# Optimization experiments

Measured on AMD Instinct MI355X. Metric: run time of the kernel, lower is better.

Reference implementation:

```python
import jax, jax.numpy as jnp
import numpy as np

B, S, D_MODEL = 4, 2048, 1024
H, DK, DV = 16, 64, 64
MASKED = False


def setup_inputs() -> dict:
    key = jax.random.key(0)
    ks = jax.random.split(key, 7)
    return {
        "q": jax.random.normal(ks[0], (B, S, D_MODEL), dtype=jnp.float32),
        "k": jax.random.normal(ks[1], (B, S, D_MODEL), dtype=jnp.float32),
        "v": jax.random.normal(ks[2], (B, S, D_MODEL), dtype=jnp.float32),
        "Wq": jax.random.normal(ks[3], (H, D_MODEL, DK), dtype=jnp.float32) * 0.05,
        "Wk": jax.random.normal(ks[4], (H, D_MODEL, DK), dtype=jnp.float32) * 0.05,
        "Wv": jax.random.normal(ks[5], (H, D_MODEL, DV), dtype=jnp.float32) * 0.05,
        "Wo": jax.random.normal(ks[6], (H * DV, D_MODEL), dtype=jnp.float32) * 0.05,
    }


def reference(q, k, v, Wq, Wk, Wv, Wo):
    # Per-head projections, batched over heads instead of a Python loop.
    Q = jnp.einsum("bsd,hdk->bhsk", q, Wq)  # [B,H,S,Dk]
    K = jnp.einsum("btd,hdk->bhtk", k, Wk)  # [B,H,S,Dk]
    V = jnp.einsum("btd,hdv->bhtv", v, Wv)  # [B,H,S,Dv]

    scale = 1.0 / jnp.sqrt(jnp.asarray(DK, dtype=Q.dtype))
    scores = jnp.einsum("bhsk,bhtk->bhst", Q, K) * scale  # [B,H,S,S]
    if MASKED:
        causal = jnp.tril(jnp.ones((S, S), dtype=bool))
        scores = jnp.where(causal, scores, jnp.finfo(scores.dtype).min)
    attn = jax.nn.softmax(scores, axis=-1)
    heads = jnp.einsum("bhst,bhtv->bhsv", attn, V)  # [B,H,S,Dv]

    # concat heads along feature dim (tf.concat(heads, axis=-1)) then Wo projection
    multi = heads.transpose(0, 2, 1, 3).reshape(q.shape[0], q.shape[1], H * DV)
    return multi @ Wo  # [B,S,D_MODEL]
```

## Files before the change

### kernel.cpp

```cpp
#include <hip/hip_runtime.h>
#include <hip/hip_bf16.h>

typedef __attribute__((ext_vector_type(8))) short short8;
typedef __attribute__((ext_vector_type(4))) short short4v;
typedef __attribute__((ext_vector_type(4))) float f32x4;
typedef __attribute__((ext_vector_type(2))) float f32x2;
typedef __attribute__((ext_vector_type(4))) unsigned short us4;
typedef __attribute__((ext_vector_type(2))) unsigned int u32x2;

#define NB 4
#define SEQ 2048
#define DMODEL 1024
#define NH 16
#define DHEAD 64
#define QSCALE 0.18033688011112042f
#define FM 34.0f

static __device__ __forceinline__ unsigned short f2bf(float f) {
    __hip_bfloat16 h = __float2bfloat16(f);
    return *reinterpret_cast<unsigned short*>(&h);
}
static __device__ __forceinline__ unsigned int cvt_pk(float lo, float hi) {
    float2 t; t.x = lo; t.y = hi;
    __hip_bfloat162 h = __float22bfloat162_rn(t);
    return *reinterpret_cast<unsigned int*>(&h);
}

typedef __attribute__((address_space(3))) unsigned int lds_u32_t;
typedef __attribute__((address_space(1))) const unsigned int glob_u32_t;
static __device__ __forceinline__ void gl_lds16(const unsigned short* g, unsigned short* l) {
    __builtin_amdgcn_global_load_lds((glob_u32_t*)g, (lds_u32_t*)l, 16, 0, 0);
}

__global__ __launch_bounds__(256) void prep_all(const float* __restrict__ q,
                                                const float* __restrict__ k,
                                                const float* __restrict__ v,
                                                const float* __restrict__ wq,
                                                const float* __restrict__ wk,
                                                const float* __restrict__ wv,
                                                const float* __restrict__ wo,
                                                unsigned short* __restrict__ xq,
                                                unsigned short* __restrict__ xk,
                                                unsigned short* __restrict__ xv,
                                                unsigned short* __restrict__ oq,
                                                unsigned short* __restrict__ ok,
                                                unsigned short* __restrict__ ov,
                                                unsigned short* __restrict__ oo) {
    const int z = blockIdx.y;
    int i = blockIdx.x * 256 + threadIdx.x;
    if (z < 3) {
        const float* in = z == 0 ? q : (z == 1 ? k : v);
        unsigned short* out = z == 0 ? xq : (z == 1 ? xk : xv);
        f32x4 val = ((const f32x4*)in)[i];
        u32x2 o;
        o.x = cvt_pk(val.x, val.y);
        o.y = cvt_pk(val.z, val.w);
        ((u32x2*)out)[i] = o;
    } else {
        if (i >= NH * DMODEL * DHEAD) return;
        if (z < 6) {
            const float* w = z == 3 ? wq : (z == 4 ? wk : wv);
            unsigned short* out = z == 3 ? oq : (z == 4 ? ok : ov);
            float scale = z == 3 ? QSCALE : 1.0f;
            int kk = i & 63;
            int d  = (i >> 6) & 1023;
            int h  = i >> 16;
            out[(size_t)(h * 64 + kk) * DMODEL + d] = f2bf(w[i] * scale);
        } else {
            int c = i & 1023;
            int r = i >> 10;
            oo[(size_t)c * 1024 + r] = f2bf(wo[i]);
        }
    }
}

struct GemmAcc { f32x4 a[4][4]; };

static __device__ __forceinline__ void gemm_core(const unsigned short* __restrict__ A,
                                                 const unsigned short* __restrict__ Bt,
                                                 unsigned short (*As)[4096],
                                                 unsigned short (*Bs)[4096],
                                                 int m0, int n0, int K, GemmAcc& acc) {
    const int tid = threadIdx.x;
    const int w = tid >> 6, l = tid & 63;
    const int lane16 = l & 15, quad = l >> 4;
    const int wr = w >> 1, wc = w & 1;

#pragma unroll
    for (int a = 0; a < 4; a++)
#pragma unroll
        for (int b = 0; b < 4; b++) acc.a[a][b] = (f32x4){0.f, 0.f, 0.f, 0.f};

    const int i0 = 2 * w, i1 = 2 * w + 1;
    const int rs = l >> 2;
    const int cc = ((l & 3) ^ ((l >> 3) & 3)) * 8;
    const unsigned short* a0 = A + (size_t)(m0 + i0 * 16 + rs) * K + cc;
    const unsigned short* a1 = A + (size_t)(m0 + i1 * 16 + rs) * K + cc;
    const unsigned short* b0 = Bt + (size_t)(n0 + i0 * 16 + rs) * K + cc;
    const unsigned short* b1 = Bt + (size_t)(n0 + i1 * 16 + rs) * K + cc;

    const int cl = (quad ^ ((lane16 >> 1) & 3)) * 8;
    const int ra = (wr * 64 + lane16) * 32 + cl;
    const int rb = (wc * 64 + lane16) * 32 + cl;

    for (int k0 = 0; k0 < K; k0 += 64) {
        __syncthreads();
#pragma unroll
        for (int h = 0; h < 2; h++) {
            gl_lds16(a0 + k0 + h * 32, &As[h][i0 * 512]);
            gl_lds16(a1 + k0 + h * 32, &As[h][i1 * 512]);
            gl_lds16(b0 + k0 + h * 32, &Bs[h][i0 * 512]);
            gl_lds16(b1 + k0 + h * 32, &Bs[h][i1 * 512]);
        }
        __syncthreads();
#pragma unroll
        for (int h = 0; h < 2; h++) {
            short8 af[4], bf[4];
#pragma unroll
            for (int mt = 0; mt < 4; mt++) af[mt] = *(const short8*)&As[h][ra + mt * 512];
#pragma unroll
            for (int nt = 0; nt < 4; nt++) bf[nt] = *(const short8*)&Bs[h][rb + nt * 512];
#pragma unroll
            for (int mt = 0; mt < 4; mt++)
#pragma unroll
                for (int nt = 0; nt < 4; nt++)
                    acc.a[mt][nt] = __builtin_amdgcn_mfma_f32_16x16x32_bf16(
                        af[mt], bf[nt], acc.a[mt][nt], 0, 0, 0);
        }
    }
}

__global__ __launch_bounds__(256) void gemm_qkv(const unsigned short* __restrict__ xq,
                                                const unsigned short* __restrict__ xk,
                                                const unsigned short* __restrict__ xv,
                                                const unsigned short* __restrict__ wq,
                                                const unsigned short* __restrict__ wk,
                                                const unsigned short* __restrict__ wv,
                                                unsigned short* __restrict__ Qb,
                                                unsigned short* __restrict__ Kb,
                                                unsigned short* __restrict__ Vtb) {
    __shared__ unsigned short As[2][4096];
    __shared__ unsigned short Bs[2][4096];
    const int z = blockIdx.z;
    const unsigned short* A = z == 0 ? xq : (z == 1 ? xk : xv);
    const unsigned short* Bt = z == 0 ? wq : (z == 1 ? wk : wv);
    unsigned short* out = z == 0 ? Qb : (z == 1 ? Kb : Vtb);

    const int m0 = blockIdx.x * 128, n0 = blockIdx.y * 128;
    GemmAcc acc;
    gemm_core(A, Bt, As, Bs, m0, n0, DMODEL, acc);

    const int l = threadIdx.x & 63, w = threadIdx.x >> 6;
    const int lane16 = l & 15, quad = l >> 4;
    const int wr = w >> 1, wc = w & 1;
    if (z < 2) {
#pragma unroll
        for (int mt = 0; mt < 4; mt++)
#pragma unroll
            for (int nt = 0; nt < 4; nt++)
#pragma unroll
                for (int r = 0; r < 4; r++) {
                    int m = m0 + wr * 64 + mt * 16 + quad * 4 + r;
                    int n = n0 + wc * 64 + nt * 16 + lane16;
                    int b_ = m >> 11, s = m & 2047, h = n >> 6, kk = n & 63;
                    out[((size_t)((b_ * NH + h) * SEQ + s) << 6) + kk] = f2bf(acc.a[mt][nt][r]);
                }
    } else {
#pragma unroll
        for (int mt = 0; mt < 4; mt++)
#pragma unroll
            for (int nt = 0; nt < 4; nt++) {
                int m = m0 + wr * 64 + mt * 16 + quad * 4;
                int n = n0 + wc * 64 + nt * 16 + lane16;
                int b_ = m >> 11, s = m & 2047, h = n >> 6, kk = n & 63;
                u32x2 pk;
                pk.x = cvt_pk(acc.a[mt][nt][0], acc.a[mt][nt][1]);
                pk.y = cvt_pk(acc.a[mt][nt][2], acc.a[mt][nt][3]);
                *(u32x2*)&out[(size_t)((b_ * NH + h) * DHEAD + kk) * SEQ + s] = pk;
            }
    }
}

__global__ __launch_bounds__(256) void gemm_out(const unsigned short* __restrict__ A,
                                                const unsigned short* __restrict__ Bt,
                                                float* __restrict__ C) {
    __shared__ unsigned short As[2][4096];
    __shared__ unsigned short Bs[2][4096];
    const int m0 = blockIdx.x * 128, n0 = blockIdx.y * 128;
    GemmAcc acc;
    gemm_core(A, Bt, As, Bs, m0, n0, DMODEL, acc);

    const int l = threadIdx.x & 63, w = threadIdx.x >> 6;
    const int lane16 = l & 15, quad = l >> 4;
    const int wr = w >> 1, wc = w & 1;
#pragma unroll
    for (int mt = 0; mt < 4; mt++)
#pragma unroll
        for (int nt = 0; nt < 4; nt++)
#pragma unroll
            for (int r = 0; r < 4; r++) {
                int m = m0 + wr * 64 + mt * 16 + quad * 4 + r;
                int n = n0 + wc * 64 + nt * 16 + lane16;
                C[(size_t)m * DMODEL + n] = acc.a[mt][nt][r];
            }
}

__global__ __launch_bounds__(256) void flash_attn(const unsigned short* __restrict__ Q,
                                                  const unsigned short* __restrict__ Kg,
                                                  const unsigned short* __restrict__ Vt,
                                                  unsigned short* __restrict__ Hout) {
    __shared__ unsigned short Ks[64 * 64];
    __shared__ unsigned short Vs[64 * 64];

    const int tid = threadIdx.x;
    const int w = tid >> 6, l = tid & 63;
    const int lane16 = l & 15, quad = l >> 4;
    const int bh = blockIdx.x & 63, b_ = bh >> 4, h = bh & 15;
    const int s0 = (blockIdx.x >> 6) * 128;

    const unsigned short* Qbh = Q + (size_t)bh * SEQ * DHEAD;
    const unsigned short* Kbh = Kg + (size_t)bh * SEQ * DHEAD;
    const unsigned short* Vbh = Vt + (size_t)bh * DHEAD * SEQ;

    short8 qf[2][2];
#pragma unroll
    for (int qm = 0; qm < 2; qm++)
#pragma unroll
        for (int ks = 0; ks < 2; ks++)
            qf[qm][ks] = *(const short8*)(Qbh +
                (size_t)(s0 + w * 32 + qm * 16 + lane16) * DHEAD + ks * 32 + quad * 8);

    f32x4 o[2][4];
#pragma unroll
    for (int qm = 0; qm < 2; qm++)
#pragma unroll
        for (int dt = 0; dt < 4; dt++) o[qm][dt] = (f32x4){0.f, 0.f, 0.f, 0.f};
    f32x2 lsum2[2];
    lsum2[0] = (f32x2){0.f, 0.f};
    lsum2[1] = (f32x2){0.f, 0.f};
    const f32x4 scinit = (f32x4){-FM, -FM, -FM, -FM};

    const int i0 = 2 * w, i1 = 2 * w + 1;
    const int rs = l >> 3;
    const int cgs = ((l & 7) ^ rs) * 8;
    const unsigned short* kg0 = Kbh + (size_t)(i0 * 8 + rs) * DHEAD + cgs;
    const unsigned short* kg1 = Kbh + (size_t)(i1 * 8 + rs) * DHEAD + cgs;
    const unsigned short* vg0 = Vbh + (size_t)(i0 * 8 + rs) * SEQ + cgs;
    const unsigned short* vg1 = Vbh + (size_t)(i1 * 8 + rs) * SEQ + cgs;
    unsigned short* lk0 = &Ks[i0 * 512];
    unsigned short* lk1 = &Ks[i1 * 512];
    unsigned short* lv0 = &Vs[i0 * 512];
    unsigned short* lv1 = &Vs[i1 * 512];

    const int swz = lane16 & 7;

    for (int t0 = 0; t0 < SEQ; t0 += 64) {
        __syncthreads();
        gl_lds16(kg0 + (size_t)t0 * DHEAD, lk0);
        gl_lds16(kg1 + (size_t)t0 * DHEAD, lk1);
        gl_lds16(vg0 + t0, lv0);
        gl_lds16(vg1 + t0, lv1);
        __syncthreads();

        short4v pf[2][4];
#pragma unroll
        for (int nt = 0; nt < 4; nt++) {
            const int kbase = (nt * 16 + lane16) * 64;
            short8 kf0 = *(const short8*)&Ks[kbase + ((quad ^ swz) * 8)];
            short8 kf1 = *(const short8*)&Ks[kbase + (((4 + quad) ^ swz) * 8)];
#pragma unroll
            for (int qm = 0; qm < 2; qm++) {
                f32x4 sc = __builtin_amdgcn_mfma_f32_16x16x32_bf16(kf0, qf[qm][0], scinit, 0, 0, 0);
                sc = __builtin_amdgcn_mfma_f32_16x16x32_bf16(kf1, qf[qm][1], sc, 0, 0, 0);
                float p0 = __builtin_amdgcn_exp2f(sc.x);
                float p1 = __builtin_amdgcn_exp2f(sc.y);
                float p2 = __builtin_amdgcn_exp2f(sc.z);
                float p3 = __builtin_amdgcn_exp2f(sc.w);
                f32x2 pa; pa.x = p0; pa.y = p1;
                f32x2 pb; pb.x = p2; pb.y = p3;
                lsum2[qm] += pa;
                lsum2[qm] += pb;
                u32x2 pk;
                pk.x = cvt_pk(p0, p1);
                pk.y = cvt_pk(p2, p3);
                pf[qm][nt] = __builtin_bit_cast(short4v, pk);
            }
        }
#pragma unroll
        for (int nt = 0; nt < 4; nt++) {
#pragma unroll
            for (int dt = 0; dt < 4; dt++) {
                int cl = (2 * nt + (quad >> 1)) ^ swz;
                short4v vf = *(const short4v*)&Vs[(dt * 16 + lane16) * 64 + cl * 8 + (quad & 1) * 4];
                o[0][dt] = __builtin_amdgcn_mfma_f32_16x16x16bf16_1k(vf, pf[0][nt], o[0][dt], 0, 0, 0);
                o[1][dt] = __builtin_amdgcn_mfma_f32_16x16x16bf16_1k(vf, pf[1][nt], o[1][dt], 0, 0, 0);
            }
        }
    }

    float lsum[2];
#pragma unroll
    for (int qm = 0; qm < 2; qm++) {
        float s = lsum2[qm].x + lsum2[qm].y;
        s += __shfl_xor(s, 16);
        s += __shfl_xor(s, 32);
        lsum[qm] = s;
    }
#pragma unroll
    for (int qm = 0; qm < 2; qm++) {
        float inv = 1.f / lsum[qm];
        int s = s0 + w * 32 + qm * 16 + lane16;
        size_t rowbase = (size_t)(b_ * SEQ + s) * DMODEL + h * 64;
#pragma unroll
        for (int dt = 0; dt < 4; dt++) {
            u32x2 ov;
            ov.x = cvt_pk(o[qm][dt][0] * inv, o[qm][dt][1] * inv);
            ov.y = cvt_pk(o[qm][dt][2] * inv, o[qm][dt][3] * inv);
            *(u32x2*)&Hout[rowbase + dt * 16 + quad * 4] = ov;
        }
    }
}

extern "C" void kernel_launch(void* const* d_in, const int* in_sizes, int n_in,
                              void* d_out, int out_size, void* d_ws, size_t ws_size,
                              hipStream_t stream) {
    const float* q  = (const float*)d_in[0];
    const float* k  = (const float*)d_in[1];
    const float* v  = (const float*)d_in[2];
    const float* Wq = (const float*)d_in[3];
    const float* Wk = (const float*)d_in[4];
    const float* Wv = (const float*)d_in[5];
    const float* Wo = (const float*)d_in[6];

    const size_t SZ_X = (size_t)NB * SEQ * DMODEL * 2;
    const size_t SZ_W = (size_t)DMODEL * DMODEL * 2;
    char* ws = (char*)d_ws;
    unsigned short* xq  = (unsigned short*)(ws);
    unsigned short* xk  = (unsigned short*)(ws + SZ_X);
    unsigned short* xv  = (unsigned short*)(ws + 2 * SZ_X);
    unsigned short* wqt = (unsigned short*)(ws + 3 * SZ_X);
    unsigned short* wkt = (unsigned short*)(ws + 3 * SZ_X + SZ_W);
    unsigned short* wvt = (unsigned short*)(ws + 3 * SZ_X + 2 * SZ_W);
    unsigned short* wot = (unsigned short*)(ws + 3 * SZ_X + 3 * SZ_W);
    unsigned short* Qb  = (unsigned short*)(ws + 3 * SZ_X + 4 * SZ_W);
    unsigned short* Kb  = (unsigned short*)(ws + 4 * SZ_X + 4 * SZ_W);
    unsigned short* Vtb = (unsigned short*)(ws + 5 * SZ_X + 4 * SZ_W);
    unsigned short* hd  = (unsigned short*)(ws + 6 * SZ_X + 4 * SZ_W);
    if (ws_size < 7 * SZ_X + 4 * SZ_W) return;

    const int n4 = NB * SEQ * DMODEL / 4;
    prep_all<<<dim3(n4 / 256, 7), 256, 0, stream>>>(q, k, v, Wq, Wk, Wv, Wo,
                                                    xq, xk, xv, wqt, wkt, wvt, wot);

    const int M = NB * SEQ;
    gemm_qkv<<<dim3(M / 128, DMODEL / 128, 3), 256, 0, stream>>>(
        xq, xk, xv, wqt, wkt, wvt, Qb, Kb, Vtb);

    flash_attn<<<dim3((SEQ / 128) * NB * NH), 256, 0, stream>>>(Qb, Kb, Vtb, hd);

    gemm_out<<<dim3(M / 128, DMODEL / 128), 256, 0, stream>>>(hd, wot, (float*)d_out);
}
```

Baseline: 357.9 us.

## Double-buffer K/V tiles in flash attention and remap block order

Adds a second LDS buffer for K and V so the next tile's global-to-LDS load is issued before computing on the current tile, overlapping memory latency with MFMA work and using one barrier per tile instead of two. It also remaps the block index so that consecutive blocks are spread across (batch, head) groups, which changes L2 locality across XCDs. This doubles LDS use per block, which may reduce occupancy, and relies on manual waitcnt/barrier ordering.

```diff
diff --git a/kernel.cpp b/kernel.cpp
--- a/kernel.cpp
+++ b/kernel.cpp
@@ -209,14 +209,15 @@
                                                   const unsigned short* __restrict__ Kg,
                                                   const unsigned short* __restrict__ Vt,
                                                   unsigned short* __restrict__ Hout) {
-    __shared__ unsigned short Ks[64 * 64];
-    __shared__ unsigned short Vs[64 * 64];
+    __shared__ unsigned short Ks[2][4096];
+    __shared__ unsigned short Vs[2][4096];
 
     const int tid = threadIdx.x;
     const int w = tid >> 6, l = tid & 63;
     const int lane16 = l & 15, quad = l >> 4;
-    const int bh = blockIdx.x & 63, b_ = bh >> 4, h = bh & 15;
-    const int s0 = (blockIdx.x >> 6) * 128;
+    const int wg = ((blockIdx.x & 7) << 7) | (blockIdx.x >> 3);
+    const int bh = wg >> 4, b_ = bh >> 4, h = bh & 15;
+    const int s0 = (wg & 15) * 128;
 
     const unsigned short* Qbh = Q + (size_t)bh * SEQ * DHEAD;
     const unsigned short* Kbh = Kg + (size_t)bh * SEQ * DHEAD;
@@ -247,27 +248,26 @@
     const unsigned short* kg1 = Kbh + (size_t)(i1 * 8 + rs) * DHEAD + cgs;
     const unsigned short* vg0 = Vbh + (size_t)(i0 * 8 + rs) * SEQ + cgs;
     const unsigned short* vg1 = Vbh + (size_t)(i1 * 8 + rs) * SEQ + cgs;
-    unsigned short* lk0 = &Ks[i0 * 512];
-    unsigned short* lk1 = &Ks[i1 * 512];
-    unsigned short* lv0 = &Vs[i0 * 512];
-    unsigned short* lv1 = &Vs[i1 * 512];
 
     const int swz = lane16 & 7;
 
-    for (int t0 = 0; t0 < SEQ; t0 += 64) {
-        __syncthreads();
-        gl_lds16(kg0 + (size_t)t0 * DHEAD, lk0);
-        gl_lds16(kg1 + (size_t)t0 * DHEAD, lk1);
-        gl_lds16(vg0 + t0, lv0);
-        gl_lds16(vg1 + t0, lv1);
-        __syncthreads();
-
+#define STAGE(B, T)                                            \
+    do {                                                       \
+        const size_t ko_ = (size_t)(T) * (64 * DHEAD);         \
+        const int vo_ = (T) * 64;                              \
+        gl_lds16(kg0 + ko_, &Ks[B][i0 * 512]);                 \
+        gl_lds16(kg1 + ko_, &Ks[B][i1 * 512]);                 \
+        gl_lds16(vg0 + vo_, &Vs[B][i0 * 512]);                 \
+        gl_lds16(vg1 + vo_, &Vs[B][i1 * 512]);                 \
+    } while (0)
+
+    auto compute = [&](const unsigned short* kb, const unsigned short* vb) {
         short4v pf[2][4];
 #pragma unroll
         for (int nt = 0; nt < 4; nt++) {
             const int kbase = (nt * 16 + lane16) * 64;
-            short8 kf0 = *(const short8*)&Ks[kbase + ((quad ^ swz) * 8)];
-            short8 kf1 = *(const short8*)&Ks[kbase + (((4 + quad) ^ swz) * 8)];
+            short8 kf0 = *(const short8*)&kb[kbase + ((quad ^ swz) * 8)];
+            short8 kf1 = *(const short8*)&kb[kbase + (((4 + quad) ^ swz) * 8)];
 #pragma unroll
             for (int qm = 0; qm < 2; qm++) {
                 f32x4 sc = __builtin_amdgcn_mfma_f32_16x16x32_bf16(kf0, qf[qm][0], scinit, 0, 0, 0);
@@ -291,12 +291,34 @@
 #pragma unroll
             for (int dt = 0; dt < 4; dt++) {
                 int cl = (2 * nt + (quad >> 1)) ^ swz;
-                short4v vf = *(const short4v*)&Vs[(dt * 16 + lane16) * 64 + cl * 8 + (quad & 1) * 4];
+                short4v vf = *(const short4v*)&vb[(dt * 16 + lane16) * 64 + cl * 8 + (quad & 1) * 4];
                 o[0][dt] = __builtin_amdgcn_mfma_f32_16x16x16bf16_1k(vf, pf[0][nt], o[0][dt], 0, 0, 0);
                 o[1][dt] = __builtin_amdgcn_mfma_f32_16x16x16bf16_1k(vf, pf[1][nt], o[1][dt], 0, 0, 0);
             }
         }
-    }
+    };
+
+    STAGE(0, 0);
+    asm volatile("s_waitcnt vmcnt(0)" ::: "memory");
+    __builtin_amdgcn_s_barrier();
+
+    const int NT = SEQ / 64;
+    for (int t = 0; t < NT; t += 2) {
+        STAGE(1, t + 1);
+        asm volatile("" ::: "memory");
+        compute(Ks[0], Vs[0]);
+        asm volatile("" ::: "memory");
+        asm volatile("s_waitcnt vmcnt(0)" ::: "memory");
+        __builtin_amdgcn_s_barrier();
+
+        if (t + 2 < NT) STAGE(0, t + 2);
+        asm volatile("" ::: "memory");
+        compute(Ks[1], Vs[1]);
+        asm volatile("" ::: "memory");
+        asm volatile("s_waitcnt vmcnt(0)" ::: "memory");
+        __builtin_amdgcn_s_barrier();
+    }
+#undef STAGE
 
     float lsum[2];
 #pragma unroll
```

Result: no change. 355.3 us (-0.7%).
